# Kernel tuning notes

Hardware: AMD Instinct MI355X
Metric: run time of the kernel (lower is better)

Reference implementation:

```python
import jax, jax.numpy as jnp
import numpy as np

NNODE = 500000       # nodes -> 2*NNODE global DOFs
NELEM = 500000       # elements, 8 DOF each (2D quad)
NDOF = 2 * NNODE


def setup_inputs() -> dict:
    key = jax.random.key(0)
    k1, k2, k3, k4 = jax.random.split(key, 4)
    u = jax.random.normal(k1, (NDOF,), dtype=jnp.float32)
    weight1 = jax.random.normal(k2, (NDOF,), dtype=jnp.float32)
    bc_idx = jnp.arange(NDOF, dtype=jnp.int64)  # free-DOF indices (all free)
    # elemental DOF map: 8 global DOF indices per element (irregular)
    edof = jax.random.randint(k3, (NELEM, 8), 0, NDOF, dtype=jnp.int64)
    # per-element 8x8 stiffness matrices
    stiffness = jax.random.normal(k4, (NELEM, 8, 8), dtype=jnp.float32)
    return {"u": u, "weight1": weight1, "bc_idx": bc_idx,
            "edof": edof, "stiffness": stiffness}


def reference(u, weight1, bc_idx, edof, stiffness):
    # u1 = zeros; u1[bc_idx] = weight1 * u[bc_idx]
    u1 = jnp.zeros_like(u).at[bc_idx].set(weight1 * u[bc_idx])
    # gather elemental DOF values: [E, 8]
    ue = u1[edof]
    # per-element stiffness matvec: [E, 8]
    fe = jnp.einsum('eij,ej->ei', stiffness, ue)
    # scatter-add assembly into global force vector
    F = jnp.zeros_like(u).at[edof.reshape(-1)].add(fe.reshape(-1))
    return F
```

## Files before the change

### kernel.cpp

```cpp
#include <hip/hip_runtime.h>

typedef float          vfloat4  __attribute__((ext_vector_type(4)));
typedef int            vint4    __attribute__((ext_vector_type(4)));
typedef unsigned int   vuint4   __attribute__((ext_vector_type(4)));

#define BSHIFT 12
#define BSIZE  4096
#define NBMAX  256
#define TPBC   512
#define RPT    8
#define BATCH  (TPBC * RPT)
#define CAP    28
#define OCAP   192
#define CAPB   20480
#define TPB    256

__global__ void scatter_u1_kernel(const float* __restrict__ u,
                                  const float* __restrict__ w1,
                                  const int* __restrict__ bc,
                                  float* __restrict__ u1, int n,
                                  int* __restrict__ gpos) {
    if (blockIdx.x == 0 && threadIdx.x < NBMAX) gpos[threadIdx.x] = 0;
    int k = blockIdx.x * blockDim.x + threadIdx.x;
    if (k < n) {
        int idx = bc[k];
        u1[idx] = w1[k] * u[idx];
    }
}

__global__ __launch_bounds__(TPBC, 8)
void compute_scatter_kernel(const float* __restrict__ u1,
                            const int* __restrict__ edof,
                            const float* __restrict__ stiff,
                            int* __restrict__ gpos,
                            unsigned int* __restrict__ pairs,
                            int total, int nb) {
    __shared__ unsigned int lstage[NBMAX * CAP];
    __shared__ int c[NBMAX];
    __shared__ int gb[NBMAX];
    __shared__ int spos[NBMAX + 1];
    __shared__ unsigned long long oflow[OCAP];
    __shared__ int noflow;

    int tid = threadIdx.x;
    int k0  = blockIdx.x * BATCH;

    int idxs[RPT];
    #pragma unroll
    for (int r = 0; r < RPT; ++r) {
        int k = k0 + r * TPBC + tid;
        idxs[r] = (k < total) ? __builtin_nontemporal_load(edof + k) : 0;
    }

    if (tid < NBMAX) c[tid] = 0;
    if (tid == 0) noflow = 0;

    float ues[RPT];
    #pragma unroll
    for (int r = 0; r < RPT; ++r) ues[r] = u1[idxs[r]];

    __syncthreads();

    #pragma unroll
    for (int h = 0; h < 2; ++h) {
        #pragma unroll
        for (int r2 = 0; r2 < RPT / 2; ++r2) {
            int r = h * (RPT / 2) + r2;
            int k = k0 + r * TPBC + tid;
            if (k < total) {
                int e = k >> 3;
                int i = k & 7;
                const vfloat4* Kr = (const vfloat4*)(stiff + (size_t)e * 64 + (size_t)i * 8);
                vfloat4 ka = __builtin_nontemporal_load(Kr);
                vfloat4 kb = __builtin_nontemporal_load(Kr + 1);
                float ue = ues[r];
                float fe;
                fe  = ka.x * __shfl(ue, 0, 8);
                fe += ka.y * __shfl(ue, 1, 8);
                fe += ka.z * __shfl(ue, 2, 8);
                fe += ka.w * __shfl(ue, 3, 8);
                fe += kb.x * __shfl(ue, 4, 8);
                fe += kb.y * __shfl(ue, 5, 8);
                fe += kb.z * __shfl(ue, 6, 8);
                fe += kb.w * __shfl(ue, 7, 8);

                unsigned short hu = __builtin_bit_cast(unsigned short, (_Float16)fe);
                int idx = idxs[r];
                unsigned int ent = ((unsigned)(idx & (BSIZE - 1)) << 16) | (unsigned)hu;
                int b  = idx >> BSHIFT;
                int rk = atomicAdd(&c[b], 1);
                if (rk < CAP) {
                    lstage[b * CAP + rk] = ent;
                } else {
                    int o = atomicAdd(&noflow, 1);
                    if (o < OCAP)
                        oflow[o] = ((unsigned long long)(((unsigned)b << 16) | (unsigned)rk) << 32)
                                 | (unsigned long long)ent;
                }
            }
        }
    }
    __syncthreads();

    if (tid < nb) gb[tid] = atomicAdd(&gpos[tid], c[tid]);
    if (tid < 64) {
        int v[4];
        int s = 0;
        for (int j = 0; j < 4; ++j) {
            int b = tid * 4 + j;
            v[j] = (b < nb) ? min(c[b], CAP) : 0;
            s += v[j];
        }
        int incl = s;
        for (int off = 1; off < 64; off <<= 1) {
            int n = __shfl_up(incl, off, 64);
            if (tid >= off) incl += n;
        }
        int run = incl - s;
        for (int j = 0; j < 4; ++j) { spos[tid * 4 + j] = run; run += v[j]; }
        if (tid == 63) spos[NBMAX] = incl;
    }
    __syncthreads();

    int S = spos[nb];
    for (int t = tid; t < S; t += TPBC) {
        int lo = 0, hi = nb;
        while (hi - lo > 1) {
            int mid = (lo + hi) >> 1;
            if (spos[mid] <= t) lo = mid; else hi = mid;
        }
        int r = t - spos[lo];
        pairs[(size_t)lo * CAPB + gb[lo] + r] = lstage[lo * CAP + r];
    }
    int no = min(noflow, OCAP);
    for (int t = tid; t < no; t += TPBC) {
        unsigned long long w2 = oflow[t];
        unsigned int en  = (unsigned int)w2;
        unsigned int hi2 = (unsigned int)(w2 >> 32);
        int b = (int)(hi2 >> 16);
        int r = (int)(hi2 & 0xffffu);
        pairs[(size_t)b * CAPB + gb[b] + r] = en;
    }
}

__global__ void bucket_reduce_kernel(const unsigned int* __restrict__ pairs,
                                     const int* __restrict__ gpos,
                                     float* __restrict__ F, int ndof) {
    __shared__ float acc[BSIZE];
    int b = blockIdx.x;
    for (int j = threadIdx.x; j < BSIZE; j += 1024) acc[j] = 0.0f;
    __syncthreads();
    int len = gpos[b];
    size_t base = (size_t)b * CAPB;
    int len4 = len & ~3;
    for (int k = threadIdx.x * 4; k < len4; k += 1024 * 4) {
        vuint4 p = __builtin_nontemporal_load((const vuint4*)(pairs + base + k));
        atomicAdd(&acc[p.x >> 16], (float)__builtin_bit_cast(_Float16, (unsigned short)(p.x & 0xffffu)));
        atomicAdd(&acc[p.y >> 16], (float)__builtin_bit_cast(_Float16, (unsigned short)(p.y & 0xffffu)));
        atomicAdd(&acc[p.z >> 16], (float)__builtin_bit_cast(_Float16, (unsigned short)(p.z & 0xffffu)));
        atomicAdd(&acc[p.w >> 16], (float)__builtin_bit_cast(_Float16, (unsigned short)(p.w & 0xffffu)));
    }
    for (int k = len4 + threadIdx.x; k < len; k += 1024) {
        unsigned p = pairs[base + k];
        atomicAdd(&acc[p >> 16], (float)__builtin_bit_cast(_Float16, (unsigned short)(p & 0xffffu)));
    }
    __syncthreads();
    int gbase = b << BSHIFT;
    for (int j = threadIdx.x; j < BSIZE; j += 1024) {
        int g = gbase + j;
        if (g < ndof) F[g] = acc[j];
    }
}

__global__ void elem_assemble_kernel(const float* __restrict__ u1,
                                     const int* __restrict__ edof,
                                     const float* __restrict__ stiff,
                                     float* __restrict__ F, int nelem) {
    int t = blockIdx.x * blockDim.x + threadIdx.x;
    int e = t >> 3;
    if (e >= nelem) return;
    int i = t & 7;
    int idx = __builtin_nontemporal_load(edof + t);
    float ue = u1[idx];
    const vfloat4* Kr = (const vfloat4*)(stiff + (size_t)e * 64 + (size_t)i * 8);
    vfloat4 k0 = __builtin_nontemporal_load(Kr);
    vfloat4 k1 = __builtin_nontemporal_load(Kr + 1);
    float fe;
    fe  = k0.x * __shfl(ue, 0, 8);
    fe += k0.y * __shfl(ue, 1, 8);
    fe += k0.z * __shfl(ue, 2, 8);
    fe += k0.w * __shfl(ue, 3, 8);
    fe += k1.x * __shfl(ue, 4, 8);
    fe += k1.y * __shfl(ue, 5, 8);
    fe += k1.z * __shfl(ue, 6, 8);
    fe += k1.w * __shfl(ue, 7, 8);
    unsafeAtomicAdd(&F[idx], fe);
}

extern "C" void kernel_launch(void* const* d_in, const int* in_sizes, int n_in,
                              void* d_out, int out_size, void* d_ws, size_t ws_size,
                              hipStream_t stream) {
    const float* u     = (const float*)d_in[0];
    const float* w1    = (const float*)d_in[1];
    const int*   bc    = (const int*)d_in[2];
    const int*   edof  = (const int*)d_in[3];
    const float* stiff = (const float*)d_in[4];
    float* F = (float*)d_out;

    int ndof  = in_sizes[0];
    int nbc   = in_sizes[2];
    int total = in_sizes[3];
    int nelem = total / 8;
    int nb    = (ndof + BSIZE - 1) >> BSHIFT;

    char* w = (char*)d_ws;
    size_t o = 0;
    auto take = [&](size_t nbytes) -> char* {
        char* p = w + o;
        o += (nbytes + 255) & ~(size_t)255;
        return p;
    };
    float* u1 = (float*)take((size_t)ndof * 4);
    unsigned int* pairs = (unsigned int*)take((size_t)nb * CAPB * 4);
    int* gpos = (int*)take((size_t)NBMAX * 4);

    (void)hipMemsetAsync(u1, 0, (size_t)ndof * sizeof(float), stream);
    scatter_u1_kernel<<<(nbc + TPB - 1) / TPB, TPB, 0, stream>>>(u, w1, bc, u1, nbc, gpos);

    if (o <= ws_size && nb <= NBMAX && total % 8 == 0) {
        int grid = (total + BATCH - 1) / BATCH;
        compute_scatter_kernel<<<grid, TPBC, 0, stream>>>(
            u1, edof, stiff, gpos, pairs, total, nb);
        bucket_reduce_kernel<<<nb, 1024, 0, stream>>>(pairs, gpos, F, ndof);
    } else {
        (void)hipMemsetAsync(F, 0, (size_t)ndof * sizeof(float), stream);
        elem_assemble_kernel<<<(total + TPB - 1) / TPB, TPB, 0, stream>>>(
            u1, edof, stiff, F, nelem);
    }
}
```

Before: 261.3 us.

## Split each bucket reduction across multiple blocks with global atomic merge

```diff
diff --git a/kernel.cpp b/kernel.cpp
--- a/kernel.cpp
+++ b/kernel.cpp
@@ -13,6 +13,8 @@
 #define CAP    28
 #define OCAP   192
 #define CAPB   20480
+#define RSPLIT 4
+#define RTPB   512
 #define TPB    256
 
 __global__ void scatter_u1_kernel(const float* __restrict__ u,
@@ -143,32 +145,41 @@
     }
 }
 
-__global__ void bucket_reduce_kernel(const unsigned int* __restrict__ pairs,
-                                     const int* __restrict__ gpos,
-                                     float* __restrict__ F, int ndof) {
+__global__ __launch_bounds__(RTPB, 4)
+void bucket_reduce_kernel(const unsigned int* __restrict__ pairs,
+                          const int* __restrict__ gpos,
+                          float* __restrict__ F, int ndof) {
     __shared__ float acc[BSIZE];
-    int b = blockIdx.x;
-    for (int j = threadIdx.x; j < BSIZE; j += 1024) acc[j] = 0.0f;
+    int b = blockIdx.x / RSPLIT;
+    int s = blockIdx.x - b * RSPLIT;
+    for (int j = threadIdx.x; j < BSIZE; j += RTPB) acc[j] = 0.0f;
     __syncthreads();
     int len = gpos[b];
-    size_t base = (size_t)b * CAPB;
-    int len4 = len & ~3;
-    for (int k = threadIdx.x * 4; k < len4; k += 1024 * 4) {
-        vuint4 p = __builtin_nontemporal_load((const vuint4*)(pairs + base + k));
-        atomicAdd(&acc[p.x >> 16], (float)__builtin_bit_cast(_Float16, (unsigned short)(p.x & 0xffffu)));
-        atomicAdd(&acc[p.y >> 16], (float)__builtin_bit_cast(_Float16, (unsigned short)(p.y & 0xffffu)));
-        atomicAdd(&acc[p.z >> 16], (float)__builtin_bit_cast(_Float16, (unsigned short)(p.z & 0xffffu)));
-        atomicAdd(&acc[p.w >> 16], (float)__builtin_bit_cast(_Float16, (unsigned short)(p.w & 0xffffu)));
-    }
-    for (int k = len4 + threadIdx.x; k < len; k += 1024) {
-        unsigned p = pairs[base + k];
-        atomicAdd(&acc[p >> 16], (float)__builtin_bit_cast(_Float16, (unsigned short)(p & 0xffffu)));
+    int per = (((len + RSPLIT - 1) / RSPLIT) + 3) & ~3;
+    int k0 = s * per;
+    int k1 = min(k0 + per, len);
+    size_t base = (size_t)b * CAPB + k0;
+    int n  = k1 - k0;
+    if (n > 0) {
+        int n4 = n & ~3;
+        for (int k = threadIdx.x * 4; k < n4; k += RTPB * 4) {
+            vuint4 p = *(const vuint4*)(pairs + base + k);
+            atomicAdd(&acc[p.x >> 16], (float)__builtin_bit_cast(_Float16, (unsigned short)(p.x & 0xffffu)));
+            atomicAdd(&acc[p.y >> 16], (float)__builtin_bit_cast(_Float16, (unsigned short)(p.y & 0xffffu)));
+            atomicAdd(&acc[p.z >> 16], (float)__builtin_bit_cast(_Float16, (unsigned short)(p.z & 0xffffu)));
+            atomicAdd(&acc[p.w >> 16], (float)__builtin_bit_cast(_Float16, (unsigned short)(p.w & 0xffffu)));
+        }
+        for (int k = n4 + threadIdx.x; k < n; k += RTPB) {
+            unsigned p = pairs[base + k];
+            atomicAdd(&acc[p >> 16], (float)__builtin_bit_cast(_Float16, (unsigned short)(p & 0xffffu)));
+        }
     }
     __syncthreads();
     int gbase = b << BSHIFT;
-    for (int j = threadIdx.x; j < BSIZE; j += 1024) {
+    for (int j = threadIdx.x; j < BSIZE; j += RTPB) {
         int g = gbase + j;
-        if (g < ndof) F[g] = acc[j];
+        float v = acc[j];
+        if (g < ndof && v != 0.0f) unsafeAtomicAdd(&F[g], v);
     }
 }
 
@@ -225,15 +236,15 @@
     int* gpos = (int*)take((size_t)NBMAX * 4);
 
     (void)hipMemsetAsync(u1, 0, (size_t)ndof * sizeof(float), stream);
+    (void)hipMemsetAsync(F, 0, (size_t)ndof * sizeof(float), stream);
     scatter_u1_kernel<<<(nbc + TPB - 1) / TPB, TPB, 0, stream>>>(u, w1, bc, u1, nbc, gpos);
 
     if (o <= ws_size && nb <= NBMAX && total % 8 == 0) {
         int grid = (total + BATCH - 1) / BATCH;
         compute_scatter_kernel<<<grid, TPBC, 0, stream>>>(
             u1, edof, stiff, gpos, pairs, total, nb);
-        bucket_reduce_kernel<<<nb, 1024, 0, stream>>>(pairs, gpos, F, ndof);
+        bucket_reduce_kernel<<<nb * RSPLIT, RTPB, 0, stream>>>(pairs, gpos, F, ndof);
     } else {
-        (void)hipMemsetAsync(F, 0, (size_t)ndof * sizeof(float), stream);
         elem_assemble_kernel<<<(total + TPB - 1) / TPB, TPB, 0, stream>>>(
             u1, edof, stiff, F, nelem);
     }
```

After: 269.7 us. 1.03x slower.
